# Kernel tuning notes

Hardware: AMD Instinct MI355X
Metric: run time of the kernel (lower is better)

The kernel has to match this reference:

```python
import jax, jax.numpy as jnp
import numpy as np

R_EPS = 1e-15

def _sdf_net(x, W1, b1, W2, b2):
    h = jax.nn.relu(x @ W1 + b1)
    return h @ W2 + b2  # [..., 1+feat]

def _fd_gradient(x, W1, b1, W2, b2, eps):
    # central finite differences of the SDF along the 3 axes
    offs = eps * jnp.eye(3, dtype=x.dtype)              # [3,3]
    xp = x[None, :, :] + offs[:, None, :]               # [3,P,3]
    xm = x[None, :, :] - offs[:, None, :]
    sp = _sdf_net(xp, W1, b1, W2, b2)[..., 0]           # [3,P]
    sm = _sdf_net(xm, W1, b1, W2, b2)[..., 0]
    return ((sp - sm) / (2.0 * eps)).T                  # [P,3]

def _softplus100(x):
    # torch.nn.Softplus(beta=100)
    return jax.nn.softplus(100.0 * x) / 100.0

def _exclusive_cumprod(a):
    ones = jnp.ones_like(a[:, :1])
    return jnp.cumprod(jnp.concatenate([ones, a], -1), -1)[:, :-1]

def _sample_pdf(bins, weights, n_samples):
    # bins [R,K], weights [R,K-1]; deterministic inverse-CDF sampling (det=True)
    weights = weights + 1e-5
    pdf = weights / jnp.sum(weights, -1, keepdims=True)
    cdf = jnp.cumsum(pdf, -1)
    cdf = jnp.concatenate([jnp.zeros_like(cdf[:, :1]), cdf], -1)  # [R,K]
    K = cdf.shape[-1]
    u = jnp.linspace(0.5 / n_samples, 1.0 - 0.5 / n_samples, n_samples, dtype=bins.dtype)
    u = jnp.broadcast_to(u[None], (bins.shape[0], n_samples))
    inds = jax.vmap(lambda c, uu: jnp.searchsorted(c, uu, side='right'))(cdf, u)
    below = jnp.clip(inds - 1, 0, K - 1)
    above = jnp.clip(inds, 0, K - 1)
    cdf_b = jnp.take_along_axis(cdf, below, -1)
    cdf_a = jnp.take_along_axis(cdf, above, -1)
    bin_b = jnp.take_along_axis(bins, below, -1)
    bin_a = jnp.take_along_axis(bins, above, -1)
    denom = cdf_a - cdf_b
    denom = jnp.where(denom < 1e-5, jnp.ones_like(denom), denom)
    t = (u - cdf_b) / denom
    return bin_b + t * (bin_a - bin_b)

def _forward(rays_o, rays_d, W1, b1, W2, b2, Wc1, bc1, Wc2, bc2, inv_s_param,
             num_steps, upsample_steps, bound):
    B, N = rays_o.shape[:2]
    ro = rays_o.reshape(-1, 3)
    rd = rays_d.reshape(-1, 3)
    R = ro.shape[0]
    bnd = float(bound)
    # near/far from cube bound
    tmin = (-bnd - ro) / (rd + R_EPS)
    tmax = (bnd - ro) / (rd + R_EPS)
    near = jnp.max(jnp.minimum(tmin, tmax), -1, keepdims=True)
    far = jnp.min(jnp.maximum(tmin, tmax), -1, keepdims=True)
    near = jnp.maximum(near, 0.05)
    z = jnp.linspace(0.0, 1.0, num_steps, dtype=ro.dtype)[None]
    z_vals = near + (far - near) * z                     # [R,S0]
    sample_dist = (far - near) / num_steps               # [R,1]
    pts = ro[:, None, :] + rd[:, None, :] * z_vals[..., None]
    pts = jnp.clip(pts, -bnd, bnd)
    # --- coarse SDF pass + inverse-CDF importance resampling (torch.no_grad) ---
    sdf_c = _sdf_net(pts.reshape(-1, 3), W1, b1, W2, b2)[:, 0].reshape(R, num_steps)
    sdf_c = jax.lax.stop_gradient(sdf_c)
    d_c = z_vals[:, 1:] - z_vals[:, :-1]
    mid_sdf = 0.5 * (sdf_c[:, 1:] + sdf_c[:, :-1])
    cos_val = jnp.clip((sdf_c[:, 1:] - sdf_c[:, :-1]) / (d_c + 1e-5), -1e3, 0.0)
    prev_c = jax.nn.sigmoid((mid_sdf - cos_val * d_c * 0.5) * 64.0)
    next_c = jax.nn.sigmoid((mid_sdf + cos_val * d_c * 0.5) * 64.0)
    alpha_c = jnp.clip((prev_c - next_c + 1e-5) / (prev_c + 1e-5), 0.0, 1.0)
    w_c = alpha_c * _exclusive_cumprod(1.0 - alpha_c + 1e-7)
    new_z = jax.lax.stop_gradient(_sample_pdf(z_vals, w_c, upsample_steps))
    z_vals = jnp.sort(jnp.concatenate([z_vals, new_z], -1), -1)
    S = num_steps + upsample_steps
    # --- fine pass: deltas / midpoints / shading / NeuS compositing ---
    deltas = z_vals[:, 1:] - z_vals[:, :-1]
    deltas = jnp.concatenate([deltas, jnp.broadcast_to(sample_dist, (R, 1))], -1)
    z_mid = jnp.concatenate([z_vals[:, :-1] + 0.5 * deltas[:, :-1], z_vals[:, -1:]], -1)
    new_pts = ro[:, None, :] + rd[:, None, :] * z_mid[..., None]
    new_pts = jnp.clip(new_pts, -bnd, bnd)
    flat_pts = new_pts.reshape(-1, 3)                    # [R*S,3]
    out = _sdf_net(flat_pts, W1, b1, W2, b2)
    sdf = out[:, :1]
    feat = out[:, 1:]
    grad = _fd_gradient(flat_pts, W1, b1, W2, b2, 0.005)  # eps=0.005*(1-ratio), ratio=0
    normal = grad / (1e-5 + jnp.linalg.norm(grad, axis=-1, keepdims=True))
    dirs = jnp.broadcast_to(rd[:, None, :], new_pts.shape).reshape(-1, 3)
    cin = jnp.concatenate([flat_pts, dirs, normal, feat], -1)
    color = jax.nn.sigmoid(jax.nn.relu(cin @ Wc1 + bc1) @ Wc2 + bc2)   # [R*S,3]
    inv_s = jnp.exp(10.0 * inv_s_param)                   # forward_variance()
    true_cos = jnp.sum(dirs * normal, -1, keepdims=True)
    iter_cos = -_softplus100(-true_cos)                   # cos_anneal_ratio = 1.0
    d_flat = deltas.reshape(-1, 1)
    prev_cdf = jax.nn.sigmoid((sdf - iter_cos * d_flat * 0.5) * inv_s)
    next_cdf = jax.nn.sigmoid((sdf + iter_cos * d_flat * 0.5) * inv_s)
    alpha = jnp.clip((prev_cdf - next_cdf + 1e-5) / (prev_cdf + 1e-5), 0.0, 1.0).reshape(R, S)
    weights = alpha * _exclusive_cumprod(1.0 - alpha + 1e-7)
    weights_sum = jnp.sum(weights, -1, keepdims=True)
    image = jnp.sum(color.reshape(R, S, 3) * weights[..., None], 1)
    image = image + (1.0 - weights_sum) * 1.0             # bg_color = 1
    return image.reshape(B, N, 3)

def setup_inputs() -> dict:
    key = jax.random.key(0)
    ks = jax.random.split(key, 8)
    B, N, H, F = 1, 4096, 64, 64
    rays_o = (jax.random.uniform(ks[0], (B, N, 3), jnp.float32) - 0.5) * 0.5
    d = jax.random.normal(ks[1], (B, N, 3), jnp.float32)
    rays_d = d / (1e-8 + jnp.linalg.norm(d, axis=-1, keepdims=True))
    def lin(k, i, o):
        return jax.random.normal(k, (i, o), jnp.float32) / np.sqrt(i).astype(np.float32)
    W1 = lin(ks[2], 3, H); b1 = jnp.zeros((H,), jnp.float32)
    W2 = lin(ks[3], H, 1 + F); b2 = jnp.zeros((1 + F,), jnp.float32)
    Wc1 = lin(ks[4], 9 + F, H); bc1 = jnp.zeros((H,), jnp.float32)
    Wc2 = lin(ks[5], H, 3); bc2 = jnp.zeros((3,), jnp.float32)
    inv_s_param = jnp.full((1,), 0.3, jnp.float32)
    return {"rays_o": rays_o, "rays_d": rays_d, "W1": W1, "b1": b1, "W2": W2, "b2": b2,
            "Wc1": Wc1, "bc1": bc1, "Wc2": Wc2, "bc2": bc2, "inv_s_param": inv_s_param,
            "num_steps": 64, "upsample_steps": 64, "bound": 1}

def reference(rays_o, rays_d, W1, b1, W2, b2, Wc1, bc1, Wc2, bc2, inv_s_param,
              num_steps, upsample_steps, bound):
    return _forward(rays_o, rays_d, W1, b1, W2, b2, Wc1, bc1, Wc2, bc2, inv_s_param,
                    num_steps, upsample_steps, bound)
```

## Files before the change

### kernel.cpp

```cpp
#include <hip/hip_runtime.h>
#include <hip/hip_bf16.h>
#include <cmath>

#define RAYS_PER_BLOCK 2
#define KS 84

#define OFF_W1    0
#define OFF_W1E   256
#define OFF_W1S   512
#define OFF_WC2   768
#define OFF_BC2   1024
#define OFF_AF    1028

typedef __attribute__((ext_vector_type(4))) short  short4v;
typedef __attribute__((ext_vector_type(8))) short  short8v;
typedef __attribute__((ext_vector_type(16))) float f32x16;

__device__ __forceinline__ float sigm(float x){ return 1.0f/(1.0f + expf(-x)); }
__device__ __forceinline__ float clampf(float x, float lo, float hi){ return fminf(fmaxf(x, lo), hi); }
__device__ __forceinline__ unsigned short f2bf(float x){
  __hip_bfloat16 h = __float2bfloat16(x);
  return *reinterpret_cast<unsigned short*>(&h);
}
__device__ __forceinline__ unsigned pk2(float a, float b){
  return (unsigned)f2bf(a) | ((unsigned)f2bf(b) << 16);
}
__device__ __forceinline__ short8v lds_load8(const unsigned short* p){
  short4v lo = *(const short4v*)p;
  short4v hi = *(const short4v*)(p + 4);
  short8v r;
  r[0]=lo[0]; r[1]=lo[1]; r[2]=lo[2]; r[3]=lo[3];
  r[4]=hi[0]; r[5]=hi[1]; r[6]=hi[2]; r[7]=hi[3];
  return r;
}

__global__ __launch_bounds__(256)
void prep_weights(const float* __restrict__ W1, const float* __restrict__ b1,
                  const float* __restrict__ W2, const float* __restrict__ b2,
                  const float* __restrict__ Wc1, const float* __restrict__ bc1,
                  const float* __restrict__ Wc2, const float* __restrict__ bc2,
                  float* __restrict__ ws)
{
  __shared__ float sWc1[64*64];
  __shared__ float sW2[64*64];
  __shared__ float sB2[64];
  const int tid = threadIdx.x;
  for (int i = tid; i < 4096; i += 256){
    int r = i >> 6, c = i & 63;
    sWc1[i] = Wc1[(9+r)*64 + c];
    sW2[i]  = W2[r*65 + 1 + c];
  }
  if (tid < 64) sB2[tid] = b2[1+tid];
  __syncthreads();

  int g = blockIdx.x * 256 + tid;
  if (g < 640){
    int f = g >> 6, ln = g & 63;
    int mb = f / 5, kk = f - 5*mb;
    int c  = 32*mb + (ln & 31);
    int kbase = 16*kk + 8*(ln >> 5);
    unsigned short* dst = ((unsigned short*)(ws + OFF_AF)) + (size_t)g * 8;
    if (kk < 4){
      float acc[8];
      #pragma unroll
      for (int j = 0; j < 8; ++j) acc[j] = 0.f;
      for (int t = 0; t < 64; ++t){
        float wv = sWc1[t*64 + c];
        #pragma unroll
        for (int j = 0; j < 8; ++j) acc[j] += sW2[(kbase+j)*64 + t] * wv;
      }
      #pragma unroll
      for (int j = 0; j < 8; ++j) dst[j] = f2bf(acc[j]);
    } else {
      for (int j = 0; j < 8; ++j){
        int k = kbase + j;
        float v;
        if (k < 73){
          v = Wc1[(k-64)*64 + c];
        } else if (k == 73){
          v = bc1[c];
          for (int t = 0; t < 64; ++t) v += sB2[t] * sWc1[t*64 + c];
        } else v = 0.f;
        dst[j] = f2bf(v);
      }
    }
  } else if (g < 704){
    int j = g - 640;
    ws[OFF_W1 + 4*j + 0] = W1[j];
    ws[OFF_W1 + 4*j + 1] = W1[64+j];
    ws[OFF_W1 + 4*j + 2] = W1[128+j];
    ws[OFF_W1 + 4*j + 3] = b1[j];
  } else if (g < 768){
    int j = g - 704;
    ws[OFF_W1E + 4*j + 0] = 0.01f * fabsf(W1[j]);
    ws[OFF_W1E + 4*j + 1] = 0.01f * fabsf(W1[64+j]);
    ws[OFF_W1E + 4*j + 2] = 0.01f * fabsf(W1[128+j]);
    ws[OFF_W1E + 4*j + 3] = W2[j*65];
  } else if (g < 832){
    int j = g - 768;
    float w2 = W2[j*65];
    ws[OFF_W1S + 4*j + 0] = (W1[j]     < 0.f) ? -w2 : w2;
    ws[OFF_W1S + 4*j + 1] = (W1[64+j]  < 0.f) ? -w2 : w2;
    ws[OFF_W1S + 4*j + 2] = (W1[128+j] < 0.f) ? -w2 : w2;
    ws[OFF_W1S + 4*j + 3] = 0.f;
  } else if (g < 896){
    int j = g - 832;
    ws[OFF_WC2 + 4*j + 0] = Wc2[j*3+0];
    ws[OFF_WC2 + 4*j + 1] = Wc2[j*3+1];
    ws[OFF_WC2 + 4*j + 2] = Wc2[j*3+2];
    ws[OFF_WC2 + 4*j + 3] = 0.f;
  } else if (g < 900){
    int j = g - 896;
    ws[OFF_BC2 + j] = (j < 3) ? bc2[j] : b2[0];
  }
}

__global__ __launch_bounds__(256)
void neus_render(const float* __restrict__ rays_o, const float* __restrict__ rays_d,
                 const float* __restrict__ inv_s_p, const float* __restrict__ ws,
                 float* __restrict__ out)
{
  __shared__ unsigned short s_aext[4][64*KS];
  __shared__ float4 s_wc2[64];
  __shared__ float  s_z[RAYS_PER_BLOCK][64];
  __shared__ float  s_cdf[RAYS_PER_BLOCK][64];
  __shared__ float  s_newz[RAYS_PER_BLOCK][64];
  __shared__ float  s_zall[RAYS_PER_BLOCK][128];
  __shared__ float  s_red[RAYS_PER_BLOCK][2][4];
  __shared__ float  s_wtot[RAYS_PER_BLOCK][2];

  const int tid  = threadIdx.x;
  const int rs   = tid >> 7;
  const int lt   = tid & 127;
  const int lane = tid & 63;
  const int wir  = (tid >> 6) & 1;
  const int wv   = tid >> 6;
  const int ray  = blockIdx.x * RAYS_PER_BLOCK + rs;

  const float4* __restrict__ pW1  = (const float4*)(ws + OFF_W1);
  const float4* __restrict__ pW1E = (const float4*)(ws + OFF_W1E);
  const float4* __restrict__ pW1S = (const float4*)(ws + OFF_W1S);
  const float*  __restrict__ pbc2 = ws + OFF_BC2;
  const float b20 = pbc2[3];

  if (tid < 64) s_wc2[tid] = ((const float4*)(ws + OFF_WC2))[tid];

  float ox = rays_o[ray*3], oy = rays_o[ray*3+1], oz = rays_o[ray*3+2];
  float dx = rays_d[ray*3], dy = rays_d[ray*3+1], dz = rays_d[ray*3+2];
  float tnx = (-1.f-ox)/(dx+1e-15f), tfx = (1.f-ox)/(dx+1e-15f);
  float tny = (-1.f-oy)/(dy+1e-15f), tfy = (1.f-oy)/(dy+1e-15f);
  float tnz = (-1.f-oz)/(dz+1e-15f), tfz = (1.f-oz)/(dz+1e-15f);
  float nearv = fmaxf(fmaxf(fminf(tnx,tfx), fminf(tny,tfy)), fminf(tnz,tfz));
  float farv  = fminf(fminf(fmaxf(tnx,tfx), fmaxf(tny,tfy)), fmaxf(tnz,tfz));
  nearv = fmaxf(nearv, 0.05f);
  const float sd = (farv - nearv) * (1.f/64.f);

  if (wir == 0){
    float zt = nearv + (farv-nearv) * ((float)lane * (1.f/63.f));
    float px = clampf(ox + dx*zt, -1.f, 1.f);
    float py = clampf(oy + dy*zt, -1.f, 1.f);
    float pz = clampf(oz + dz*zt, -1.f, 1.f);
    float acc = b20;
    #pragma unroll 8
    for (int j = 0; j < 64; ++j){
      float4 w = pW1[j];
      acc += fmaxf(px*w.x + py*w.y + pz*w.z + w.w, 0.f) * ws[OFF_W1E + 4*j + 3];
    }
    s_z[rs][lane] = zt;
    float s1  = __shfl_down(acc, 1);
    float zt1 = nearv + (farv-nearv) * ((float)(lane+1) * (1.f/63.f));
    float a_c = 0.f, qv = 1.f;
    if (lane < 63){
      float dc   = zt1 - zt;
      float mid  = 0.5f*(acc + s1);
      float cosv = clampf((s1-acc)/(dc+1e-5f), -1000.f, 0.f);
      float est  = cosv*dc*0.5f;
      float pcv  = sigm((mid-est)*64.f);
      float ncv  = sigm((mid+est)*64.f);
      a_c = clampf((pcv-ncv+1e-5f)/(pcv+1e-5f), 0.f, 1.f);
      qv  = 1.f - a_c + 1e-7f;
    }
    float p = qv;
    #pragma unroll
    for (int off = 1; off < 64; off <<= 1){
      float t = __shfl_up(p, off);
      if (lane >= off) p *= t;
    }
    float ec = __shfl_up(p, 1);
    if (lane == 0) ec = 1.f;
    float wvv = (lane < 63) ? (a_c*ec + 1e-5f) : 0.f;
    float tot = wvv;
    #pragma unroll
    for (int off = 32; off > 0; off >>= 1) tot += __shfl_xor(tot, off);
    float cs = wvv;
    #pragma unroll
    for (int off = 1; off < 64; off <<= 1){
      float t = __shfl_up(cs, off);
      if (lane >= off) cs += t;
    }
    if (lane == 0)  s_cdf[rs][0] = 0.f;
    if (lane < 63)  s_cdf[rs][lane+1] = cs / tot;
  }
  __syncthreads();

  if (wir == 0){
    float u = ((float)lane + 0.5f) * (1.f/64.f);
    int lo = 0, hi = 64;
    while (lo < hi){
      int m = (lo+hi) >> 1;
      if (s_cdf[rs][m] <= u) lo = m+1; else hi = m;
    }
    int below = lo - 1;
    int above = lo < 63 ? lo : 63;
    float cb = s_cdf[rs][below], ca = s_cdf[rs][above];
    float bb = s_z[rs][below],   ba = s_z[rs][above];
    float den = ca - cb; if (den < 1e-5f) den = 1.f;
    float tt = (u - cb)/den;
    s_newz[rs][lane] = bb + tt*(ba - bb);
  }
  __syncthreads();

  const short8v* pAF = (const short8v*)(ws + OFF_AF);
  short8v af[10];
  #pragma unroll
  for (int f = 0; f < 10; ++f) af[f] = pAF[f*64 + lane];

  {
    float v; int pos;
    if (lt < 64){
      v = s_z[rs][lt];
      int lo = 0, hi = 64;
      while (lo < hi){ int m=(lo+hi)>>1; if (s_newz[rs][m] < v) lo = m+1; else hi = m; }
      pos = lt + lo;
    } else {
      int jj = lt - 64;
      v = s_newz[rs][jj];
      int lo = 0, hi = 64;
      while (lo < hi){ int m=(lo+hi)>>1; if (s_z[rs][m] <= v) lo = m+1; else hi = m; }
      pos = jj + lo;
    }
    s_zall[rs][pos] = v;
  }
  __syncthreads();

  float zc = s_zall[rs][lt];
  float zn = s_zall[rs][lt < 127 ? lt+1 : 127];
  float delta = (lt < 127) ? (zn - zc) : sd;
  float zm    = (lt < 127) ? (zc + 0.5f*delta) : zc;
  float px = clampf(ox + dx*zm, -1.f, 1.f);
  float py = clampf(oy + dy*zm, -1.f, 1.f);
  float pz = clampf(oz + dz*zm, -1.f, 1.f);

  unsigned short* arow = &s_aext[wv][(unsigned)lane * KS];
  float sa = b20;
  float gxa = 0.f, gya = 0.f, gza = 0.f;
  #pragma unroll 2
  for (int j2 = 0; j2 < 32; ++j2){
    int j = 2*j2;
    float4 w0 = pW1[j],   e0 = pW1E[j],   s0 = pW1S[j];
    float4 w1 = pW1[j+1], e1 = pW1E[j+1], s1v = pW1S[j+1];
    float base0 = fmaf(px, w0.x, fmaf(py, w0.y, fmaf(pz, w0.z, w0.w)));
    float base1 = fmaf(px, w1.x, fmaf(py, w1.y, fmaf(pz, w1.z, w1.w)));
    float hv0 = fmaxf(base0, 0.f), hv1 = fmaxf(base1, 0.f);
    sa = fmaf(hv0, e0.w, sa); sa = fmaf(hv1, e1.w, sa);
    gxa = fmaf(__builtin_amdgcn_fmed3f(fmaf(0.5f, e0.x, base0), 0.f, e0.x), s0.x, gxa);
    gya = fmaf(__builtin_amdgcn_fmed3f(fmaf(0.5f, e0.y, base0), 0.f, e0.y), s0.y, gya);
    gza = fmaf(__builtin_amdgcn_fmed3f(fmaf(0.5f, e0.z, base0), 0.f, e0.z), s0.z, gza);
    gxa = fmaf(__builtin_amdgcn_fmed3f(fmaf(0.5f, e1.x, base1), 0.f, e1.x), s1v.x, gxa);
    gya = fmaf(__builtin_amdgcn_fmed3f(fmaf(0.5f, e1.y, base1), 0.f, e1.y), s1v.y, gya);
    gza = fmaf(__builtin_amdgcn_fmed3f(fmaf(0.5f, e1.z, base1), 0.f, e1.z), s1v.z, gza);
    *(unsigned*)&arow[j] = pk2(hv0, hv1);
  }
  float sdfv = sa;
  float gx = gxa*100.f, gy = gya*100.f, gz = gza*100.f;
  float gn = 1e-5f + sqrtf(gx*gx + gy*gy + gz*gz);
  float nx = gx/gn, ny = gy/gn, nz = gz/gn;

  *(unsigned*)&arow[64] = pk2(px, py);
  *(unsigned*)&arow[66] = pk2(pz, dx);
  *(unsigned*)&arow[68] = pk2(dy, dz);
  *(unsigned*)&arow[70] = pk2(nx, ny);
  *(unsigned*)&arow[72] = pk2(nz, 1.0f);
  *(unsigned*)&arow[74] = 0u;
  *(unsigned*)&arow[76] = 0u;
  *(unsigned*)&arow[78] = 0u;

  __builtin_amdgcn_wave_barrier();

  f32x16 acc00, acc01, acc10, acc11;
  #pragma unroll
  for (int i = 0; i < 16; ++i){ acc00[i]=0.f; acc01[i]=0.f; acc10[i]=0.f; acc11[i]=0.f; }
  const unsigned short* aw = s_aext[wv];
  const int scol = lane & 31;
  const int half8 = (lane >> 5) * 8;
  #pragma unroll
  for (int kk = 0; kk < 5; ++kk){
    int koff = 16*kk + half8;
    short8v b0 = lds_load8(&aw[ scol      * KS + koff]);
    short8v b1 = lds_load8(&aw[(32+scol) * KS + koff]);
    acc00 = __builtin_amdgcn_mfma_f32_32x32x16_bf16(af[kk],   b0, acc00, 0, 0, 0);
    acc10 = __builtin_amdgcn_mfma_f32_32x32x16_bf16(af[5+kk], b0, acc10, 0, 0, 0);
    acc01 = __builtin_amdgcn_mfma_f32_32x32x16_bf16(af[kk],   b1, acc01, 0, 0, 0);
    acc11 = __builtin_amdgcn_mfma_f32_32x32x16_bf16(af[5+kk], b1, acc11, 0, 0, 0);
  }

  float pr0=0.f,pr1=0.f,pr2=0.f,pr3=0.f,pr4=0.f,pr5=0.f;
  const int halfoff = (lane >> 5) * 4;
  #pragma unroll
  for (int r = 0; r < 16; ++r){
    int ci = (r & 3) + 8*(r >> 2) + halfoff;
    float4 wA = s_wc2[ci];
    float4 wB = s_wc2[32 + ci];
    float v;
    v = fmaxf(acc00[r], 0.f); pr0 = fmaf(v, wA.x, pr0); pr1 = fmaf(v, wA.y, pr1); pr2 = fmaf(v, wA.z, pr2);
    v = fmaxf(acc10[r], 0.f); pr0 = fmaf(v, wB.x, pr0); pr1 = fmaf(v, wB.y, pr1); pr2 = fmaf(v, wB.z, pr2);
    v = fmaxf(acc01[r], 0.f); pr3 = fmaf(v, wA.x, pr3); pr4 = fmaf(v, wA.y, pr4); pr5 = fmaf(v, wA.z, pr5);
    v = fmaxf(acc11[r], 0.f); pr3 = fmaf(v, wB.x, pr3); pr4 = fmaf(v, wB.y, pr4); pr5 = fmaf(v, wB.z, pr5);
  }
  pr0 += __shfl_xor(pr0, 32); pr1 += __shfl_xor(pr1, 32); pr2 += __shfl_xor(pr2, 32);
  pr3 += __shfl_xor(pr3, 32); pr4 += __shfl_xor(pr4, 32); pr5 += __shfl_xor(pr5, 32);
  const bool hihalf = (lane >= 32);
  float c0 = sigm((hihalf ? pr3 : pr0) + pbc2[0]);
  float c1 = sigm((hihalf ? pr4 : pr1) + pbc2[1]);
  float c2 = sigm((hihalf ? pr5 : pr2) + pbc2[2]);

  const float inv_s = expf(10.f * inv_s_p[0]);
  float tcos = dx*nx + dy*ny + dz*nz;
  float aarg = -100.f * tcos;
  float spv  = (aarg > 0.f) ? (aarg + log1pf(expf(-aarg))) : log1pf(expf(aarg));
  float iter_cos = -(spv * 0.01f);
  float est = iter_cos * delta * 0.5f;
  float pcv = sigm((sdfv - est)*inv_s);
  float ncv = sigm((sdfv + est)*inv_s);
  float alpha = clampf((pcv - ncv + 1e-5f)/(pcv + 1e-5f), 0.f, 1.f);

  float qv = 1.f - alpha + 1e-7f;
  float p = qv;
  #pragma unroll
  for (int off = 1; off < 64; off <<= 1){
    float t = __shfl_up(p, off);
    if (lane >= off) p *= t;
  }
  if (lane == 63) s_wtot[rs][wir] = p;
  __syncthreads();
  float excl = __shfl_up(p, 1);
  if (lane == 0) excl = 1.f;
  if (wir == 1) excl *= s_wtot[rs][0];
  float w  = alpha * excl;
  float r0 = w, r1 = w*c0, r2 = w*c1, r3 = w*c2;
  #pragma unroll
  for (int off = 32; off > 0; off >>= 1){
    r0 += __shfl_xor(r0, off);
    r1 += __shfl_xor(r1, off);
    r2 += __shfl_xor(r2, off);
    r3 += __shfl_xor(r3, off);
  }
  if (lane == 0){
    s_red[rs][wir][0]=r0; s_red[rs][wir][1]=r1; s_red[rs][wir][2]=r2; s_red[rs][wir][3]=r3;
  }
  __syncthreads();
  if (lt == 0){
    float wsum = s_red[rs][0][0] + s_red[rs][1][0];
    float bg = 1.f - wsum;
    out[ray*3+0] = s_red[rs][0][1] + s_red[rs][1][1] + bg;
    out[ray*3+1] = s_red[rs][0][2] + s_red[rs][1][2] + bg;
    out[ray*3+2] = s_red[rs][0][3] + s_red[rs][1][3] + bg;
  }
}

extern "C" void kernel_launch(void* const* d_in, const int* in_sizes, int n_in,
                              void* d_out, int out_size, void* d_ws, size_t ws_size,
                              hipStream_t stream)
{
  const float* rays_o = (const float*)d_in[0];
  const float* rays_d = (const float*)d_in[1];
  const float* W1  = (const float*)d_in[2];
  const float* b1  = (const float*)d_in[3];
  const float* W2  = (const float*)d_in[4];
  const float* b2  = (const float*)d_in[5];
  const float* Wc1 = (const float*)d_in[6];
  const float* bc1 = (const float*)d_in[7];
  const float* Wc2 = (const float*)d_in[8];
  const float* bc2 = (const float*)d_in[9];
  const float* inv_s = (const float*)d_in[10];
  float* out = (float*)d_out;
  float* ws  = (float*)d_ws;

  prep_weights<<<4, 256, 0, stream>>>(W1, b1, W2, b2, Wc1, bc1, Wc2, bc2, ws);

  const int R = in_sizes[0] / 3;
  dim3 grid(R / RAYS_PER_BLOCK), block(256);
  neus_render<<<grid, block, 0, stream>>>(rays_o, rays_d, inv_s, ws, out);
}
```

Before: 130.8 us.

## Compute folded color weights with MFMA in one-block prep, hoist alpha before MLP

The weight-prep kernel now runs as a single block and computes the folded W2·Wc1 product with bf16 MFMA instructions instead of a scalar 64-long dot-product loop per thread. The result is staged in LDS and written out in the fragment layout. The render kernel also moves the alpha/transmittance scan (including its __syncthreads) ahead of the color MFMA, replacing the wave barrier, so the scan's latency can overlap with the matrix work. In exchange, the product is accumulated from bf16-rounded inputs, which changes numerics slightly, and the barrier placement shifts.

```diff
diff --git a/kernel.cpp b/kernel.cpp
--- a/kernel.cpp
+++ b/kernel.cpp
@@ -41,77 +41,90 @@
                   const float* __restrict__ Wc2, const float* __restrict__ bc2,
                   float* __restrict__ ws)
 {
-  __shared__ float sWc1[64*64];
-  __shared__ float sW2[64*64];
-  __shared__ float sB2[64];
-  const int tid = threadIdx.x;
+  __shared__ unsigned short W2T[64*KS];
+  __shared__ unsigned short ABUF[64*KS];
+  const int tid  = threadIdx.x;
+  const int lane = tid & 63;
+  const int wv   = tid >> 6;
+  const int l31  = lane & 31;
+  const int h    = lane >> 5;
+
   for (int i = tid; i < 4096; i += 256){
-    int r = i >> 6, c = i & 63;
-    sWc1[i] = Wc1[(9+r)*64 + c];
-    sW2[i]  = W2[r*65 + 1 + c];
-  }
-  if (tid < 64) sB2[tid] = b2[1+tid];
-  __syncthreads();
-
-  int g = blockIdx.x * 256 + tid;
-  if (g < 640){
-    int f = g >> 6, ln = g & 63;
-    int mb = f / 5, kk = f - 5*mb;
-    int c  = 32*mb + (ln & 31);
-    int kbase = 16*kk + 8*(ln >> 5);
-    unsigned short* dst = ((unsigned short*)(ws + OFF_AF)) + (size_t)g * 8;
-    if (kk < 4){
-      float acc[8];
-      #pragma unroll
-      for (int j = 0; j < 8; ++j) acc[j] = 0.f;
-      for (int t = 0; t < 64; ++t){
-        float wv = sWc1[t*64 + c];
-        #pragma unroll
-        for (int j = 0; j < 8; ++j) acc[j] += sW2[(kbase+j)*64 + t] * wv;
-      }
-      #pragma unroll
-      for (int j = 0; j < 8; ++j) dst[j] = f2bf(acc[j]);
-    } else {
-      for (int j = 0; j < 8; ++j){
-        int k = kbase + j;
-        float v;
-        if (k < 73){
-          v = Wc1[(k-64)*64 + c];
-        } else if (k == 73){
-          v = bc1[c];
-          for (int t = 0; t < 64; ++t) v += sB2[t] * sWc1[t*64 + c];
-        } else v = 0.f;
-        dst[j] = f2bf(v);
-      }
-    }
-  } else if (g < 704){
-    int j = g - 640;
-    ws[OFF_W1 + 4*j + 0] = W1[j];
-    ws[OFF_W1 + 4*j + 1] = W1[64+j];
-    ws[OFF_W1 + 4*j + 2] = W1[128+j];
+    int k = i >> 6, t = i & 63;
+    W2T[k*KS + t] = f2bf(W2[k*65 + 1 + t]);
+  }
+  for (int i = tid; i < 576; i += 256){
+    int ii = i >> 6, c = i & 63;
+    ABUF[c*KS + 64 + ii] = f2bf(Wc1[ii*64 + c]);
+  }
+  for (int i = tid; i < 384; i += 256){
+    int z = i >> 6, c = i & 63;
+    ABUF[c*KS + 74 + z] = 0;
+  }
+  if (wv == 3){
+    float acc = bc1[lane];
+    #pragma unroll 4
+    for (int t = 0; t < 64; ++t) acc = fmaf(b2[1+t], Wc1[(9+t)*64 + lane], acc);
+    ABUF[lane*KS + 73] = f2bf(acc);
+  }
+  if (tid < 64){
+    int j = tid;
+    float wx = W1[j], wy = W1[64+j], wz = W1[128+j];
+    float w2 = W2[j*65];
+    ws[OFF_W1 + 4*j + 0] = wx;
+    ws[OFF_W1 + 4*j + 1] = wy;
+    ws[OFF_W1 + 4*j + 2] = wz;
     ws[OFF_W1 + 4*j + 3] = b1[j];
-  } else if (g < 768){
-    int j = g - 704;
-    ws[OFF_W1E + 4*j + 0] = 0.01f * fabsf(W1[j]);
-    ws[OFF_W1E + 4*j + 1] = 0.01f * fabsf(W1[64+j]);
-    ws[OFF_W1E + 4*j + 2] = 0.01f * fabsf(W1[128+j]);
-    ws[OFF_W1E + 4*j + 3] = W2[j*65];
-  } else if (g < 832){
-    int j = g - 768;
-    float w2 = W2[j*65];
-    ws[OFF_W1S + 4*j + 0] = (W1[j]     < 0.f) ? -w2 : w2;
-    ws[OFF_W1S + 4*j + 1] = (W1[64+j]  < 0.f) ? -w2 : w2;
-    ws[OFF_W1S + 4*j + 2] = (W1[128+j] < 0.f) ? -w2 : w2;
+    ws[OFF_W1E + 4*j + 0] = 0.01f * fabsf(wx);
+    ws[OFF_W1E + 4*j + 1] = 0.01f * fabsf(wy);
+    ws[OFF_W1E + 4*j + 2] = 0.01f * fabsf(wz);
+    ws[OFF_W1E + 4*j + 3] = w2;
+    ws[OFF_W1S + 4*j + 0] = (wx < 0.f) ? -w2 : w2;
+    ws[OFF_W1S + 4*j + 1] = (wy < 0.f) ? -w2 : w2;
+    ws[OFF_W1S + 4*j + 2] = (wz < 0.f) ? -w2 : w2;
     ws[OFF_W1S + 4*j + 3] = 0.f;
-  } else if (g < 896){
-    int j = g - 832;
+  } else if (tid < 128){
+    int j = tid - 64;
     ws[OFF_WC2 + 4*j + 0] = Wc2[j*3+0];
     ws[OFF_WC2 + 4*j + 1] = Wc2[j*3+1];
     ws[OFF_WC2 + 4*j + 2] = Wc2[j*3+2];
     ws[OFF_WC2 + 4*j + 3] = 0.f;
-  } else if (g < 900){
-    int j = g - 896;
+  } else if (tid < 132){
+    int j = tid - 128;
     ws[OFF_BC2 + j] = (j < 3) ? bc2[j] : b2[0];
+  }
+  __syncthreads();
+
+  {
+    const int mb = wv & 1, kb = wv >> 1;
+    f32x16 e;
+    #pragma unroll
+    for (int i = 0; i < 16; ++i) e[i] = 0.f;
+    #pragma unroll
+    for (int s = 0; s < 4; ++s){
+      short8v afr;
+      #pragma unroll
+      for (int j = 0; j < 8; ++j)
+        afr[j] = (short)f2bf(Wc1[(9 + 16*s + 8*h + j)*64 + 32*mb + l31]);
+      short8v bfr = lds_load8(&W2T[(32*kb + l31)*KS + 16*s + 8*h]);
+      e = __builtin_amdgcn_mfma_f32_32x32x16_bf16(afr, bfr, e, 0, 0, 0);
+    }
+    const int kcol = 32*kb + l31;
+    #pragma unroll
+    for (int r = 0; r < 16; ++r){
+      int c = 32*mb + (r & 3) + 8*(r >> 2) + 4*h;
+      ABUF[c*KS + kcol] = f2bf(e[r]);
+    }
+  }
+  __syncthreads();
+
+  for (int i = tid; i < 640; i += 256){
+    int f = i >> 6, ln = i & 63;
+    int mb = f / 5, kk = f - 5*mb;
+    int c  = 32*mb + (ln & 31);
+    int kb2 = 16*kk + 8*(ln >> 5);
+    short8v v = lds_load8(&ABUF[c*KS + kb2]);
+    *((short8v*)(((unsigned short*)(ws + OFF_AF)) + (size_t)i * 8)) = v;
   }
 }
 
@@ -285,7 +298,29 @@
   *(unsigned*)&arow[76] = 0u;
   *(unsigned*)&arow[78] = 0u;
 
-  __builtin_amdgcn_wave_barrier();
+  const float inv_s = expf(10.f * inv_s_p[0]);
+  float tcos = dx*nx + dy*ny + dz*nz;
+  float aarg = -100.f * tcos;
+  float spv  = (aarg > 0.f) ? (aarg + log1pf(expf(-aarg))) : log1pf(expf(aarg));
+  float iter_cos = -(spv * 0.01f);
+  float est = iter_cos * delta * 0.5f;
+  float pcv = sigm((sdfv - est)*inv_s);
+  float ncv = sigm((sdfv + est)*inv_s);
+  float alpha = clampf((pcv - ncv + 1e-5f)/(pcv + 1e-5f), 0.f, 1.f);
+
+  float qv = 1.f - alpha + 1e-7f;
+  float p = qv;
+  #pragma unroll
+  for (int off = 1; off < 64; off <<= 1){
+    float t = __shfl_up(p, off);
+    if (lane >= off) p *= t;
+  }
+  if (lane == 63) s_wtot[rs][wir] = p;
+  __syncthreads();
+  float excl = __shfl_up(p, 1);
+  if (lane == 0) excl = 1.f;
+  if (wir == 1) excl *= s_wtot[rs][0];
+  float w  = alpha * excl;
 
   f32x16 acc00, acc01, acc10, acc11;
   #pragma unroll
@@ -324,29 +359,6 @@
   float c1 = sigm((hihalf ? pr4 : pr1) + pbc2[1]);
   float c2 = sigm((hihalf ? pr5 : pr2) + pbc2[2]);
 
-  const float inv_s = expf(10.f * inv_s_p[0]);
-  float tcos = dx*nx + dy*ny + dz*nz;
-  float aarg = -100.f * tcos;
-  float spv  = (aarg > 0.f) ? (aarg + log1pf(expf(-aarg))) : log1pf(expf(aarg));
-  float iter_cos = -(spv * 0.01f);
-  float est = iter_cos * delta * 0.5f;
-  float pcv = sigm((sdfv - est)*inv_s);
-  float ncv = sigm((sdfv + est)*inv_s);
-  float alpha = clampf((pcv - ncv + 1e-5f)/(pcv + 1e-5f), 0.f, 1.f);
-
-  float qv = 1.f - alpha + 1e-7f;
-  float p = qv;
-  #pragma unroll
-  for (int off = 1; off < 64; off <<= 1){
-    float t = __shfl_up(p, off);
-    if (lane >= off) p *= t;
-  }
-  if (lane == 63) s_wtot[rs][wir] = p;
-  __syncthreads();
-  float excl = __shfl_up(p, 1);
-  if (lane == 0) excl = 1.f;
-  if (wir == 1) excl *= s_wtot[rs][0];
-  float w  = alpha * excl;
   float r0 = w, r1 = w*c0, r2 = w*c1, r3 = w*c2;
   #pragma unroll
   for (int off = 32; off > 0; off >>= 1){
@@ -386,7 +398,7 @@
   float* out = (float*)d_out;
   float* ws  = (float*)d_ws;
 
-  prep_weights<<<4, 256, 0, stream>>>(W1, b1, W2, b2, Wc1, bc1, Wc2, bc2, ws);
+  prep_weights<<<1, 256, 0, stream>>>(W1, b1, W2, b2, Wc1, bc1, Wc2, bc2, ws);
 
   const int R = in_sizes[0] / 3;
   dim3 grid(R / RAYS_PER_BLOCK), block(256);
```

New measurement: 129.9 us. No clear change (-0.7%).
